# Performance work log

Hardware: AMD Instinct MI355X
Metric: run time of the kernel (lower is better)

## Reference

```python
import jax, jax.numpy as jnp
import numpy as np

B, S, D, H = 2, 2048, 1024, 16
DK = D // H  # 64


def setup_inputs() -> dict:
    rng = jax.random.key(0)
    ks = jax.random.split(rng, 11)
    std = 1.0 / np.sqrt(D)
    query = jax.random.normal(ks[0], (B, S, D), dtype=jnp.float32)
    key = jax.random.normal(ks[1], (B, S, D), dtype=jnp.float32)
    value = jax.random.normal(ks[2], (B, S, D), dtype=jnp.float32)
    # causal mask, broadcast over batch and heads
    mask = jnp.tril(jnp.ones((S, S), dtype=jnp.int32))[None, None]
    Wq = jax.random.normal(ks[3], (D, D), dtype=jnp.float32) * std
    bq = jnp.zeros((D,), dtype=jnp.float32)
    Wk = jax.random.normal(ks[4], (D, D), dtype=jnp.float32) * std
    bk = jnp.zeros((D,), dtype=jnp.float32)
    Wv = jax.random.normal(ks[5], (D, D), dtype=jnp.float32) * std
    bv = jnp.zeros((D,), dtype=jnp.float32)
    Wo = jax.random.normal(ks[6], (D, D), dtype=jnp.float32) * std
    bo = jnp.zeros((D,), dtype=jnp.float32)
    return {"query": query, "key": key, "value": value, "mask": mask,
            "Wq": Wq, "bq": bq, "Wk": Wk, "bk": bk,
            "Wv": Wv, "bv": bv, "Wo": Wo, "bo": bo}


def reference(query, key, value, mask, Wq, bq, Wk, bk, Wv, bv, Wo, bo):
    scale = jnp.sqrt(jnp.float32(DK))
    # linear projections (nn.Linear applies x @ W.T + b)
    Q = query @ Wq.T + bq
    K = key @ Wk.T + bk
    V = value @ Wv.T + bv
    # [B,S,D] -> [B,H,S,DK]
    Q = Q.reshape(B, S, H, DK).transpose(0, 2, 1, 3)
    K = K.reshape(B, S, H, DK).transpose(0, 2, 1, 3)
    V = V.reshape(B, S, H, DK).transpose(0, 2, 1, 3)
    scores = jnp.einsum('bhqd,bhkd->bhqk', Q, K) / scale
    scores = jnp.where(mask == 0, jnp.float32(-1e9), scores)
    attention = jax.nn.softmax(scores, axis=-1)  # dropout is identity in eval
    x = jnp.einsum('bhqk,bhkd->bhqd', attention, V)
    x = x.transpose(0, 2, 1, 3).reshape(B, S, D)
    x = x @ Wo.T + bo
    return (x, attention)
```

## Files before the change

kernel.cpp:

```cpp
#include <hip/hip_runtime.h>
#include <stdint.h>

#define S_LEN 2048
#define DMODEL 1024
#define NHEAD 16
#define DKH 64
#define NROW 4096

using short8  = __attribute__((ext_vector_type(8))) short;
using short4v = __attribute__((ext_vector_type(4))) short;
using float4v = __attribute__((ext_vector_type(4))) float;

__device__ __forceinline__ short f2bf(float f) {
    union { float f; unsigned u; } v; v.f = f;
    unsigned r = (v.u + 0x7fffu + ((v.u >> 16) & 1u)) >> 16;
    return (short)r;
}

__device__ __forceinline__ float bf2f(short b) {
    union { unsigned u; float f; } c;
    c.u = ((unsigned)(unsigned short)b) << 16;
    return c.f;
}

__device__ __forceinline__ float4v mfma16(short8 a, short8 b, float4v c) {
    return __builtin_amdgcn_mfma_f32_16x16x32_bf16(a, b, c, 0, 0, 0);
}

__device__ __forceinline__ void gload16(const short* g, short* l) {
    __builtin_amdgcn_global_load_lds(
        (const __attribute__((address_space(1))) void*)g,
        (__attribute__((address_space(3))) void*)l, 16, 0, 0);
}

__global__ __launch_bounds__(256) void convert_kernel(
    const float* __restrict__ q, const float* __restrict__ k, const float* __restrict__ v,
    const float* __restrict__ wq, const float* __restrict__ wk, const float* __restrict__ wv,
    const float* __restrict__ wo,
    short* __restrict__ oq, short* __restrict__ ok_, short* __restrict__ ov,
    short* __restrict__ owq, short* __restrict__ owk, short* __restrict__ owv,
    short* __restrict__ owo)
{
    const size_t A = (size_t)NROW * DMODEL;
    const size_t W = (size_t)DMODEL * DMODEL;
    size_t i = ((size_t)blockIdx.x * 256 + threadIdx.x) * 4;
    const float* src; short* dst; size_t off;
    if (i < A)            { src = q;  dst = oq;  off = i; }
    else if (i < 2 * A)   { src = k;  dst = ok_; off = i - A; }
    else if (i < 3 * A)   { src = v;  dst = ov;  off = i - 2 * A; }
    else {
        size_t j = i - 3 * A; int wsel = (int)(j / W); off = j % W;
        src = (wsel == 0) ? wq : (wsel == 1) ? wk : (wsel == 2) ? wv : wo;
        dst = (wsel == 0) ? owq : (wsel == 1) ? owk : (wsel == 2) ? owv : owo;
    }
    float4v x = *(const float4v*)(src + off);
    short4v o;
    o[0] = f2bf(x[0]); o[1] = f2bf(x[1]); o[2] = f2bf(x[2]); o[3] = f2bf(x[3]);
    *(short4v*)(dst + off) = o;
}

__global__ __launch_bounds__(256) void gemm_qkv(
    const short* __restrict__ Xq, const short* __restrict__ Xk, const short* __restrict__ Xv,
    const short* __restrict__ Wq, const short* __restrict__ Wk, const short* __restrict__ Wv,
    const float* __restrict__ bq, const float* __restrict__ bk, const float* __restrict__ bv,
    short* __restrict__ Qo, short* __restrict__ Ko, short* __restrict__ Vt)
{
    int zy = blockIdx.y;
    int z = zy >> 3;
    int n0 = (zy & 7) * 128;
    const short* X = (z == 0) ? Xq : (z == 1) ? Xk : Xv;
    const short* W = (z == 0) ? Wq : (z == 1) ? Wk : Wv;
    const float* bias = (z == 0) ? bq : (z == 1) ? bk : bv;
    int m0 = blockIdx.x * 128;

    __shared__ __align__(16) short As[128 * 32];
    __shared__ __align__(16) short Bs[128 * 32];

    int tid = threadIdx.x, lane = tid & 63, w = tid >> 6;
    int row_in = lane & 15, grp = lane >> 4;
    int wm = (w & 1) * 64, wn = (w >> 1) * 64;

    float4v acc[4][4];
#pragma unroll
    for (int m = 0; m < 4; m++)
#pragma unroll
        for (int n = 0; n < 4; n++) acc[m][n] = (float4v){0.f, 0.f, 0.f, 0.f};

    for (int k0 = 0; k0 < DMODEL; k0 += 32) {
#pragma unroll
        for (int j = 0; j < 2; j++) {
            int chunk = j * 256 + tid;
            int r = chunk >> 2, c = (chunk & 3) * 8;
            gload16(X + (size_t)(m0 + r) * DMODEL + k0 + c,
                    As + (size_t)(j * 256 + w * 64) * 8);
            gload16(W + (size_t)(n0 + r) * DMODEL + k0 + c,
                    Bs + (size_t)(j * 256 + w * 64) * 8);
        }
        __syncthreads();

        short8 af[4], bf[4];
#pragma unroll
        for (int m = 0; m < 4; m++)
            af[m] = *(const short8*)&As[(wm + m * 16 + row_in) * 32 + grp * 8];
#pragma unroll
        for (int n = 0; n < 4; n++)
            bf[n] = *(const short8*)&Bs[(wn + n * 16 + row_in) * 32 + grp * 8];
#pragma unroll
        for (int m = 0; m < 4; m++)
#pragma unroll
            for (int n = 0; n < 4; n++)
                acc[m][n] = mfma16(af[m], bf[n], acc[m][n]);
        __syncthreads();
    }

#pragma unroll
    for (int m = 0; m < 4; m++) {
#pragma unroll
        for (int n = 0; n < 4; n++) {
            int col = n0 + wn + n * 16 + row_in;
            int h = col >> 6, dk = col & 63;
            float bval = bias[col];
            if (z < 2) {
                short* dst = (z == 0) ? Qo : Ko;
#pragma unroll
                for (int r = 0; r < 4; r++) {
                    int rowg = m0 + wm + m * 16 + grp * 4 + r;
                    int bb = rowg >> 11, s = rowg & 2047;
                    dst[(((size_t)(bb * NHEAD + h)) * S_LEN + s) * DKH + dk] =
                        f2bf(acc[m][n][r] + bval);
                }
            } else {
                int rowg0 = m0 + wm + m * 16 + grp * 4;
                int bb = rowg0 >> 11, s0 = rowg0 & 2047;
                short4v pk;
#pragma unroll
                for (int r = 0; r < 4; r++) pk[r] = f2bf(acc[m][n][r] + bval);
                *(short4v*)(Vt + ((size_t)(bb * NHEAD + h) * DKH + dk) * S_LEN + s0) = pk;
            }
        }
    }
}

__global__ __launch_bounds__(256) void gemm_out(
    const short* __restrict__ X, const short* __restrict__ W,
    const float* __restrict__ bias, float* __restrict__ out)
{
    int m0 = blockIdx.x * 128, n0 = blockIdx.y * 128;

    __shared__ __align__(16) short As[128 * 32];
    __shared__ __align__(16) short Bs[128 * 32];

    int tid = threadIdx.x, lane = tid & 63, w = tid >> 6;
    int row_in = lane & 15, grp = lane >> 4;
    int wm = (w & 1) * 64, wn = (w >> 1) * 64;

    float4v acc[4][4];
#pragma unroll
    for (int m = 0; m < 4; m++)
#pragma unroll
        for (int n = 0; n < 4; n++) acc[m][n] = (float4v){0.f, 0.f, 0.f, 0.f};

    for (int k0 = 0; k0 < DMODEL; k0 += 32) {
#pragma unroll
        for (int j = 0; j < 2; j++) {
            int chunk = j * 256 + tid;
            int r = chunk >> 2, c = (chunk & 3) * 8;
            gload16(X + (size_t)(m0 + r) * DMODEL + k0 + c,
                    As + (size_t)(j * 256 + w * 64) * 8);
            gload16(W + (size_t)(n0 + r) * DMODEL + k0 + c,
                    Bs + (size_t)(j * 256 + w * 64) * 8);
        }
        __syncthreads();

        short8 af[4], bf[4];
#pragma unroll
        for (int m = 0; m < 4; m++)
            af[m] = *(const short8*)&As[(wm + m * 16 + row_in) * 32 + grp * 8];
#pragma unroll
        for (int n = 0; n < 4; n++)
            bf[n] = *(const short8*)&Bs[(wn + n * 16 + row_in) * 32 + grp * 8];
#pragma unroll
        for (int m = 0; m < 4; m++)
#pragma unroll
            for (int n = 0; n < 4; n++)
                acc[m][n] = mfma16(af[m], bf[n], acc[m][n]);
        __syncthreads();
    }

#pragma unroll
    for (int m = 0; m < 4; m++)
#pragma unroll
        for (int n = 0; n < 4; n++) {
            int col = n0 + wn + n * 16 + row_in;
            float bval = bias[col];
#pragma unroll
            for (int r = 0; r < 4; r++) {
                int rowg = m0 + wm + m * 16 + grp * 4 + r;
                out[(size_t)rowg * DMODEL + col] = acc[m][n][r] + bval;
            }
        }
}

__global__ __launch_bounds__(256) void attn_kernel(
    const short* __restrict__ Q, const short* __restrict__ K, const short* __restrict__ Vt,
    float* __restrict__ Attn, short* __restrict__ Xatt)
{
    int bh = blockIdx.x;
    int q0 = blockIdx.y * 64;
    int tid = threadIdx.x, lane = tid & 63, w = tid >> 6;
    int row_in = lane & 15, grp = lane >> 4;
    int qbase = q0 + w * 16;

    const short* Qh = Q + (size_t)bh * S_LEN * DKH;
    const short* Kh = K + (size_t)bh * S_LEN * DKH;
    const short* Vh = Vt + (size_t)bh * DKH * S_LEN;
    float* Ah = Attn + (size_t)bh * S_LEN * S_LEN;

    __shared__ __align__(16) short Ks[64 * 72];
    __shared__ __align__(16) short Vs[64 * 72];
    __shared__ __align__(16) short Plds[4][16 * 72];

    short8 qf0 = *(const short8*)(Qh + (size_t)(qbase + row_in) * DKH + grp * 8);
    short8 qf1 = *(const short8*)(Qh + (size_t)(qbase + row_in) * DKH + 32 + grp * 8);

    const float SC = 0.125f * 1.44269504f;
    float l[4] = {0.f, 0.f, 0.f, 0.f};
    int Tmax = q0 / 64 + 1;

    for (int t = 0; t < Tmax; t++) {
        int kv0 = t * 64;
        {
            const short* src = Kh + (size_t)kv0 * DKH;
#pragma unroll
            for (int j = 0; j < 2; j++) {
                int ch = j * 256 + tid;
                int r = ch >> 3, c = (ch & 7) * 8;
                short8 kv = *(const short8*)(src + ch * 8);
                *(short8*)&Ks[r * 72 + c] = kv;
            }
        }
        __syncthreads();
#pragma unroll
        for (int u = 0; u < 4; u++) {
            short8 b0 = *(const short8*)&Ks[(u * 16 + row_in) * 72 + grp * 8];
            short8 b1 = *(const short8*)&Ks[(u * 16 + row_in) * 72 + 32 + grp * 8];
            float4v a = (float4v){0.f, 0.f, 0.f, 0.f};
            a = mfma16(qf0, b0, a);
            a = mfma16(qf1, b1, a);
            int colg = kv0 + u * 16 + row_in;
#pragma unroll
            for (int r = 0; r < 4; r++) {
                int rowg = qbase + grp * 4 + r;
                float e = (colg > rowg) ? 0.0f : exp2f(a[r] * SC);
                l[r] += e;
            }
        }
        __syncthreads();
    }
    float rinv[4];
#pragma unroll
    for (int r = 0; r < 4; r++) {
        float s = l[r];
        s += __shfl_xor(s, 1, 64);
        s += __shfl_xor(s, 2, 64);
        s += __shfl_xor(s, 4, 64);
        s += __shfl_xor(s, 8, 64);
        rinv[r] = 1.0f / s;
    }

    float4v o[4];
#pragma unroll
    for (int v = 0; v < 4; v++) o[v] = (float4v){0.f, 0.f, 0.f, 0.f};

    for (int t = 0; t < Tmax; t++) {
        int kv0 = t * 64;
        {
            const short* srcK = Kh + (size_t)kv0 * DKH;
#pragma unroll
            for (int j = 0; j < 2; j++) {
                int ch = j * 256 + tid;
                int r = ch >> 3, c = (ch & 7) * 8;
                short8 kv = *(const short8*)(srcK + ch * 8);
                *(short8*)&Ks[r * 72 + c] = kv;
                short8 vv = *(const short8*)(Vh + (size_t)r * S_LEN + kv0 + c);
                *(short8*)&Vs[r * 72 + c] = vv;
            }
        }
        __syncthreads();
#pragma unroll
        for (int u = 0; u < 4; u++) {
            short8 b0 = *(const short8*)&Ks[(u * 16 + row_in) * 72 + grp * 8];
            short8 b1 = *(const short8*)&Ks[(u * 16 + row_in) * 72 + 32 + grp * 8];
            float4v a = (float4v){0.f, 0.f, 0.f, 0.f};
            a = mfma16(qf0, b0, a);
            a = mfma16(qf1, b1, a);
            int colg = kv0 + u * 16 + row_in;
#pragma unroll
            for (int r = 0; r < 4; r++) {
                int rowg = qbase + grp * 4 + r;
                float p = (colg > rowg) ? 0.0f : exp2f(a[r] * SC) * rinv[r];
                Plds[w][(grp * 4 + r) * 72 + u * 16 + row_in] = f2bf(p);
            }
        }
        asm volatile("s_waitcnt lgkmcnt(0)" ::: "memory");
#pragma unroll
        for (int rr = 0; rr < 4; rr++) {
            int rloc = rr * 4 + grp;
            short4v pb = *(const short4v*)&Plds[w][rloc * 72 + row_in * 4];
            float4v pf;
#pragma unroll
            for (int i = 0; i < 4; i++) pf[i] = bf2f(pb[i]);
            *(float4v*)(Ah + (size_t)(qbase + rloc) * S_LEN + kv0 + row_in * 4) = pf;
        }
        short8 pa0 = *(const short8*)&Plds[w][row_in * 72 + grp * 8];
        short8 pa1 = *(const short8*)&Plds[w][row_in * 72 + 32 + grp * 8];
#pragma unroll
        for (int v = 0; v < 4; v++) {
            short8 b0 = *(const short8*)&Vs[(v * 16 + row_in) * 72 + grp * 8];
            short8 b1 = *(const short8*)&Vs[(v * 16 + row_in) * 72 + 32 + grp * 8];
            o[v] = mfma16(pa0, b0, o[v]);
            o[v] = mfma16(pa1, b1, o[v]);
        }
        __syncthreads();
    }

    float4v zz = (float4v){0.f, 0.f, 0.f, 0.f};
    for (int kv0 = Tmax * 64; kv0 < S_LEN; kv0 += 64) {
#pragma unroll
        for (int r = 0; r < 4; r++) {
            int rowg = qbase + r * 4 + grp;
            *(float4v*)(Ah + (size_t)rowg * S_LEN + kv0 + row_in * 4) = zz;
        }
    }

    int b = bh >> 4, h = bh & 15;
#pragma unroll
    for (int v = 0; v < 4; v++) {
#pragma unroll
        for (int r = 0; r < 4; r++) {
            int s = qbase + grp * 4 + r;
            int col = h * 64 + v * 16 + row_in;
            Xatt[(size_t)(b * S_LEN + s) * DMODEL + col] = f2bf(o[v][r]);
        }
    }
}

extern "C" void kernel_launch(void* const* d_in, const int* in_sizes, int n_in,
                              void* d_out, int out_size, void* d_ws, size_t ws_size,
                              hipStream_t stream) {
    const float* q  = (const float*)d_in[0];
    const float* k  = (const float*)d_in[1];
    const float* v  = (const float*)d_in[2];
    const float* Wq = (const float*)d_in[4];
    const float* bq = (const float*)d_in[5];
    const float* Wk = (const float*)d_in[6];
    const float* bk = (const float*)d_in[7];
    const float* Wv = (const float*)d_in[8];
    const float* bv = (const float*)d_in[9];
    const float* Wo = (const float*)d_in[10];
    const float* bo = (const float*)d_in[11];

    float* out_x    = (float*)d_out;
    float* out_attn = out_x + (size_t)NROW * DMODEL;

    char* ws = (char*)d_ws;
    size_t off = 0;
    auto carve = [&](size_t bytes) -> char* {
        char* p = ws + off;
        off += (bytes + 255) & ~(size_t)255;
        return p;
    };
    const size_t XB = (size_t)NROW * DMODEL * sizeof(short);
    const size_t WB = (size_t)DMODEL * DMODEL * sizeof(short);
    short* Xq  = (short*)carve(XB);
    short* Xk  = (short*)carve(XB);
    short* Xv  = (short*)carve(XB);
    short* Wqb = (short*)carve(WB);
    short* Wkb = (short*)carve(WB);
    short* Wvb = (short*)carve(WB);
    short* Wob = (short*)carve(WB);
    short* Qb  = (short*)carve(XB);
    short* Kb  = (short*)carve(XB);
    short* Vtb = (short*)carve(XB);
    short* Xat = (short*)carve(XB);

    convert_kernel<<<dim3(16384), dim3(256), 0, stream>>>(
        q, k, v, Wq, Wk, Wv, Wo, Xq, Xk, Xv, Wqb, Wkb, Wvb, Wob);

    gemm_qkv<<<dim3(NROW / 128, 24), dim3(256), 0, stream>>>(
        Xq, Xk, Xv, Wqb, Wkb, Wvb, bq, bk, bv, Qb, Kb, Vtb);

    attn_kernel<<<dim3(32, S_LEN / 64), dim3(256), 0, stream>>>(
        Qb, Kb, Vtb, out_attn, Xat);

    gemm_out<<<dim3(NROW / 128, DMODEL / 128), dim3(256), 0, stream>>>(
        Xat, Wob, bo, out_x);
}
```

Baseline: 731.4 us.

## Fuse PV into first attention pass, drop LDS K/V staging, reverse block order

```diff
diff --git a/kernel.cpp b/kernel.cpp
--- a/kernel.cpp
+++ b/kernel.cpp
@@ -206,7 +206,7 @@
     float* __restrict__ Attn, short* __restrict__ Xatt)
 {
     int bh = blockIdx.x;
-    int q0 = blockIdx.y * 64;
+    int q0 = (int)(gridDim.y - 1 - blockIdx.y) * 64;
     int tid = threadIdx.x, lane = tid & 63, w = tid >> 6;
     int row_in = lane & 15, grp = lane >> 4;
     int qbase = q0 + w * 16;
@@ -216,47 +216,58 @@
     const short* Vh = Vt + (size_t)bh * DKH * S_LEN;
     float* Ah = Attn + (size_t)bh * S_LEN * S_LEN;
 
-    __shared__ __align__(16) short Ks[64 * 72];
-    __shared__ __align__(16) short Vs[64 * 72];
     __shared__ __align__(16) short Plds[4][16 * 72];
+    __shared__ float rinv_w[4][16];
 
     short8 qf0 = *(const short8*)(Qh + (size_t)(qbase + row_in) * DKH + grp * 8);
     short8 qf1 = *(const short8*)(Qh + (size_t)(qbase + row_in) * DKH + 32 + grp * 8);
 
     const float SC = 0.125f * 1.44269504f;
     float l[4] = {0.f, 0.f, 0.f, 0.f};
+    float4v o[4];
+#pragma unroll
+    for (int v = 0; v < 4; v++) o[v] = (float4v){0.f, 0.f, 0.f, 0.f};
     int Tmax = q0 / 64 + 1;
 
     for (int t = 0; t < Tmax; t++) {
         int kv0 = t * 64;
-        {
-            const short* src = Kh + (size_t)kv0 * DKH;
-#pragma unroll
-            for (int j = 0; j < 2; j++) {
-                int ch = j * 256 + tid;
-                int r = ch >> 3, c = (ch & 7) * 8;
-                short8 kv = *(const short8*)(src + ch * 8);
-                *(short8*)&Ks[r * 72 + c] = kv;
-            }
-        }
-        __syncthreads();
-#pragma unroll
-        for (int u = 0; u < 4; u++) {
-            short8 b0 = *(const short8*)&Ks[(u * 16 + row_in) * 72 + grp * 8];
-            short8 b1 = *(const short8*)&Ks[(u * 16 + row_in) * 72 + 32 + grp * 8];
-            float4v a = (float4v){0.f, 0.f, 0.f, 0.f};
-            a = mfma16(qf0, b0, a);
-            a = mfma16(qf1, b1, a);
+        short8 kf[8];
+#pragma unroll
+        for (int u = 0; u < 4; u++) {
+            kf[2 * u]     = *(const short8*)(Kh + (size_t)(kv0 + u * 16 + row_in) * DKH + grp * 8);
+            kf[2 * u + 1] = *(const short8*)(Kh + (size_t)(kv0 + u * 16 + row_in) * DKH + 32 + grp * 8);
+        }
+        float4v a[4];
+#pragma unroll
+        for (int u = 0; u < 4; u++) {
+            float4v acc = (float4v){0.f, 0.f, 0.f, 0.f};
+            acc = mfma16(qf0, kf[2 * u], acc);
+            acc = mfma16(qf1, kf[2 * u + 1], acc);
+            a[u] = acc;
+        }
+#pragma unroll
+        for (int u = 0; u < 4; u++) {
             int colg = kv0 + u * 16 + row_in;
 #pragma unroll
             for (int r = 0; r < 4; r++) {
                 int rowg = qbase + grp * 4 + r;
-                float e = (colg > rowg) ? 0.0f : exp2f(a[r] * SC);
+                float e = (colg > rowg) ? 0.0f : exp2f(a[u][r] * SC);
                 l[r] += e;
+                Plds[w][(grp * 4 + r) * 72 + u * 16 + row_in] = f2bf(e);
             }
         }
-        __syncthreads();
-    }
+        asm volatile("s_waitcnt lgkmcnt(0)" ::: "memory");
+        short8 pa0 = *(const short8*)&Plds[w][row_in * 72 + grp * 8];
+        short8 pa1 = *(const short8*)&Plds[w][row_in * 72 + 32 + grp * 8];
+#pragma unroll
+        for (int v = 0; v < 4; v++) {
+            short8 vb0 = *(const short8*)(Vh + (size_t)(v * 16 + row_in) * S_LEN + kv0 + grp * 8);
+            short8 vb1 = *(const short8*)(Vh + (size_t)(v * 16 + row_in) * S_LEN + kv0 + 32 + grp * 8);
+            o[v] = mfma16(pa0, vb0, o[v]);
+            o[v] = mfma16(pa1, vb1, o[v]);
+        }
+    }
+
     float rinv[4];
 #pragma unroll
     for (int r = 0; r < 4; r++) {
@@ -267,61 +278,60 @@
         s += __shfl_xor(s, 8, 64);
         rinv[r] = 1.0f / s;
     }
-
-    float4v o[4];
-#pragma unroll
-    for (int v = 0; v < 4; v++) o[v] = (float4v){0.f, 0.f, 0.f, 0.f};
+    if (row_in == 0) {
+#pragma unroll
+        for (int r = 0; r < 4; r++) rinv_w[w][grp * 4 + r] = rinv[r];
+    }
+
+    int b = bh >> 4, h = bh & 15;
+#pragma unroll
+    for (int v = 0; v < 4; v++) {
+#pragma unroll
+        for (int r = 0; r < 4; r++) {
+            int s = qbase + grp * 4 + r;
+            int col = h * 64 + v * 16 + row_in;
+            Xatt[(size_t)(b * S_LEN + s) * DMODEL + col] = f2bf(o[v][r] * rinv[r]);
+        }
+    }
+    asm volatile("s_waitcnt lgkmcnt(0)" ::: "memory");
 
     for (int t = 0; t < Tmax; t++) {
         int kv0 = t * 64;
-        {
-            const short* srcK = Kh + (size_t)kv0 * DKH;
-#pragma unroll
-            for (int j = 0; j < 2; j++) {
-                int ch = j * 256 + tid;
-                int r = ch >> 3, c = (ch & 7) * 8;
-                short8 kv = *(const short8*)(srcK + ch * 8);
-                *(short8*)&Ks[r * 72 + c] = kv;
-                short8 vv = *(const short8*)(Vh + (size_t)r * S_LEN + kv0 + c);
-                *(short8*)&Vs[r * 72 + c] = vv;
-            }
-        }
-        __syncthreads();
-#pragma unroll
-        for (int u = 0; u < 4; u++) {
-            short8 b0 = *(const short8*)&Ks[(u * 16 + row_in) * 72 + grp * 8];
-            short8 b1 = *(const short8*)&Ks[(u * 16 + row_in) * 72 + 32 + grp * 8];
-            float4v a = (float4v){0.f, 0.f, 0.f, 0.f};
-            a = mfma16(qf0, b0, a);
-            a = mfma16(qf1, b1, a);
+        short8 kf[8];
+#pragma unroll
+        for (int u = 0; u < 4; u++) {
+            kf[2 * u]     = *(const short8*)(Kh + (size_t)(kv0 + u * 16 + row_in) * DKH + grp * 8);
+            kf[2 * u + 1] = *(const short8*)(Kh + (size_t)(kv0 + u * 16 + row_in) * DKH + 32 + grp * 8);
+        }
+        float4v a[4];
+#pragma unroll
+        for (int u = 0; u < 4; u++) {
+            float4v acc = (float4v){0.f, 0.f, 0.f, 0.f};
+            acc = mfma16(qf0, kf[2 * u], acc);
+            acc = mfma16(qf1, kf[2 * u + 1], acc);
+            a[u] = acc;
+        }
+#pragma unroll
+        for (int u = 0; u < 4; u++) {
             int colg = kv0 + u * 16 + row_in;
 #pragma unroll
             for (int r = 0; r < 4; r++) {
                 int rowg = qbase + grp * 4 + r;
-                float p = (colg > rowg) ? 0.0f : exp2f(a[r] * SC) * rinv[r];
-                Plds[w][(grp * 4 + r) * 72 + u * 16 + row_in] = f2bf(p);
+                float e = (colg > rowg) ? 0.0f : exp2f(a[u][r] * SC);
+                Plds[w][(grp * 4 + r) * 72 + u * 16 + row_in] = f2bf(e);
             }
         }
         asm volatile("s_waitcnt lgkmcnt(0)" ::: "memory");
 #pragma unroll
         for (int rr = 0; rr < 4; rr++) {
             int rloc = rr * 4 + grp;
+            float rv = rinv_w[w][rloc];
             short4v pb = *(const short4v*)&Plds[w][rloc * 72 + row_in * 4];
             float4v pf;
 #pragma unroll
-            for (int i = 0; i < 4; i++) pf[i] = bf2f(pb[i]);
-            *(float4v*)(Ah + (size_t)(qbase + rloc) * S_LEN + kv0 + row_in * 4) = pf;
-        }
-        short8 pa0 = *(const short8*)&Plds[w][row_in * 72 + grp * 8];
-        short8 pa1 = *(const short8*)&Plds[w][row_in * 72 + 32 + grp * 8];
-#pragma unroll
-        for (int v = 0; v < 4; v++) {
-            short8 b0 = *(const short8*)&Vs[(v * 16 + row_in) * 72 + grp * 8];
-            short8 b1 = *(const short8*)&Vs[(v * 16 + row_in) * 72 + 32 + grp * 8];
-            o[v] = mfma16(pa0, b0, o[v]);
-            o[v] = mfma16(pa1, b1, o[v]);
-        }
-        __syncthreads();
+            for (int i = 0; i < 4; i++) pf[i] = bf2f(pb[i]) * rv;
+            *(float4v*)(Ah + (size_t)(q0 + rloc + ((w * 16))) * S_LEN + kv0 + row_in * 4) = pf;
+        }
     }
 
     float4v zz = (float4v){0.f, 0.f, 0.f, 0.f};
@@ -330,17 +340,6 @@
         for (int r = 0; r < 4; r++) {
             int rowg = qbase + r * 4 + grp;
             *(float4v*)(Ah + (size_t)rowg * S_LEN + kv0 + row_in * 4) = zz;
-        }
-    }
-
-    int b = bh >> 4, h = bh & 15;
-#pragma unroll
-    for (int v = 0; v < 4; v++) {
-#pragma unroll
-        for (int r = 0; r < 4; r++) {
-            int s = qbase + grp * 4 + r;
-            int col = h * 64 + v * 16 + row_in;
-            Xatt[(size_t)(b * S_LEN + s) * DMODEL + col] = f2bf(o[v][r]);
         }
     }
 }
```

Result: slower. 866.2 us (+18.4%).

## Fuse softmax passes by deferring normalization to a separate rescale kernel

Applied to the files above, without the earlier changes.

```diff
diff --git a/kernel.cpp b/kernel.cpp
--- a/kernel.cpp
+++ b/kernel.cpp
@@ -203,10 +203,10 @@
 
 __global__ __launch_bounds__(256) void attn_kernel(
     const short* __restrict__ Q, const short* __restrict__ K, const short* __restrict__ Vt,
-    float* __restrict__ Attn, short* __restrict__ Xatt)
+    float* __restrict__ rinvg, float* __restrict__ Attn, short* __restrict__ Xatt)
 {
     int bh = blockIdx.x;
-    int q0 = blockIdx.y * 64;
+    int q0 = (int)(gridDim.y - 1 - blockIdx.y) * 64;
     int tid = threadIdx.x, lane = tid & 63, w = tid >> 6;
     int row_in = lane & 15, grp = lane >> 4;
     int qbase = q0 + w * 16;
@@ -225,52 +225,10 @@
 
     const float SC = 0.125f * 1.44269504f;
     float l[4] = {0.f, 0.f, 0.f, 0.f};
+    float4v o[4];
+#pragma unroll
+    for (int v = 0; v < 4; v++) o[v] = (float4v){0.f, 0.f, 0.f, 0.f};
     int Tmax = q0 / 64 + 1;
-
-    for (int t = 0; t < Tmax; t++) {
-        int kv0 = t * 64;
-        {
-            const short* src = Kh + (size_t)kv0 * DKH;
-#pragma unroll
-            for (int j = 0; j < 2; j++) {
-                int ch = j * 256 + tid;
-                int r = ch >> 3, c = (ch & 7) * 8;
-                short8 kv = *(const short8*)(src + ch * 8);
-                *(short8*)&Ks[r * 72 + c] = kv;
-            }
-        }
-        __syncthreads();
-#pragma unroll
-        for (int u = 0; u < 4; u++) {
-            short8 b0 = *(const short8*)&Ks[(u * 16 + row_in) * 72 + grp * 8];
-            short8 b1 = *(const short8*)&Ks[(u * 16 + row_in) * 72 + 32 + grp * 8];
-            float4v a = (float4v){0.f, 0.f, 0.f, 0.f};
-            a = mfma16(qf0, b0, a);
-            a = mfma16(qf1, b1, a);
-            int colg = kv0 + u * 16 + row_in;
-#pragma unroll
-            for (int r = 0; r < 4; r++) {
-                int rowg = qbase + grp * 4 + r;
-                float e = (colg > rowg) ? 0.0f : exp2f(a[r] * SC);
-                l[r] += e;
-            }
-        }
-        __syncthreads();
-    }
-    float rinv[4];
-#pragma unroll
-    for (int r = 0; r < 4; r++) {
-        float s = l[r];
-        s += __shfl_xor(s, 1, 64);
-        s += __shfl_xor(s, 2, 64);
-        s += __shfl_xor(s, 4, 64);
-        s += __shfl_xor(s, 8, 64);
-        rinv[r] = 1.0f / s;
-    }
-
-    float4v o[4];
-#pragma unroll
-    for (int v = 0; v < 4; v++) o[v] = (float4v){0.f, 0.f, 0.f, 0.f};
 
     for (int t = 0; t < Tmax; t++) {
         int kv0 = t * 64;
@@ -298,8 +256,9 @@
 #pragma unroll
             for (int r = 0; r < 4; r++) {
                 int rowg = qbase + grp * 4 + r;
-                float p = (colg > rowg) ? 0.0f : exp2f(a[r] * SC) * rinv[r];
-                Plds[w][(grp * 4 + r) * 72 + u * 16 + row_in] = f2bf(p);
+                float e = (colg > rowg) ? 0.0f : exp2f(a[r] * SC);
+                l[r] += e;
+                Plds[w][(grp * 4 + r) * 72 + u * 16 + row_in] = f2bf(e);
             }
         }
         asm volatile("s_waitcnt lgkmcnt(0)" ::: "memory");
@@ -324,6 +283,22 @@
         __syncthreads();
     }
 
+    float rinv[4];
+#pragma unroll
+    for (int r = 0; r < 4; r++) {
+        float s = l[r];
+        s += __shfl_xor(s, 1, 64);
+        s += __shfl_xor(s, 2, 64);
+        s += __shfl_xor(s, 4, 64);
+        s += __shfl_xor(s, 8, 64);
+        rinv[r] = 1.0f / s;
+    }
+    if (row_in == 0) {
+#pragma unroll
+        for (int r = 0; r < 4; r++)
+            rinvg[(size_t)bh * S_LEN + qbase + grp * 4 + r] = rinv[r];
+    }
+
     float4v zz = (float4v){0.f, 0.f, 0.f, 0.f};
     for (int kv0 = Tmax * 64; kv0 < S_LEN; kv0 += 64) {
 #pragma unroll
@@ -340,8 +315,26 @@
         for (int r = 0; r < 4; r++) {
             int s = qbase + grp * 4 + r;
             int col = h * 64 + v * 16 + row_in;
-            Xatt[(size_t)(b * S_LEN + s) * DMODEL + col] = f2bf(o[v][r]);
-        }
+            Xatt[(size_t)(b * S_LEN + s) * DMODEL + col] = f2bf(o[v][r] * rinv[r]);
+        }
+    }
+}
+
+__global__ __launch_bounds__(256) void attn_norm_kernel(
+    const float* __restrict__ rinvg, float* __restrict__ Attn)
+{
+    int bh = blockIdx.x;
+    int strip = (int)(gridDim.y - 1 - blockIdx.y);
+    int tid = threadIdx.x;
+    int row = strip * 64 + (tid >> 2);
+    int q4 = (tid & 3) * 4;
+    float* Ah = Attn + (size_t)bh * S_LEN * S_LEN + (size_t)row * S_LEN;
+    float rv = rinvg[(size_t)bh * S_LEN + row];
+    int ncol = (strip + 1) * 64;
+    for (int c = q4; c < ncol; c += 16) {
+        float4v v = *(float4v*)(Ah + c);
+        v[0] *= rv; v[1] *= rv; v[2] *= rv; v[3] *= rv;
+        *(float4v*)(Ah + c) = v;
     }
 }
 
@@ -383,6 +376,7 @@
     short* Kb  = (short*)carve(XB);
     short* Vtb = (short*)carve(XB);
     short* Xat = (short*)carve(XB);
+    float* Rin = (float*)carve((size_t)2 * NHEAD * S_LEN * sizeof(float));
 
     convert_kernel<<<dim3(16384), dim3(256), 0, stream>>>(
         q, k, v, Wq, Wk, Wv, Wo, Xq, Xk, Xv, Wqb, Wkb, Wvb, Wob);
@@ -391,8 +385,11 @@
         Xq, Xk, Xv, Wqb, Wkb, Wvb, bq, bk, bv, Qb, Kb, Vtb);
 
     attn_kernel<<<dim3(32, S_LEN / 64), dim3(256), 0, stream>>>(
-        Qb, Kb, Vtb, out_attn, Xat);
+        Qb, Kb, Vtb, Rin, out_attn, Xat);
 
     gemm_out<<<dim3(NROW / 128, DMODEL / 128), dim3(256), 0, stream>>>(
         Xat, Wob, bo, out_x);
-}
+
+    attn_norm_kernel<<<dim3(32, 32), dim3(256), 0, stream>>>(
+        Rin, out_attn);
+}
```

New measurement: 971.1 us. 1.33x slower.
